# Kernel tuning notes

Measured on AMD Instinct MI355X. Metric: run time of the kernel, lower is better.

The kernel has to match this reference:

```python
import jax, jax.numpy as jnp
import numpy as np
from jax import lax

B, CIN, H, W = 32, 128, 64, 64
COUT, K, NK, HID = 128, 3, 4, 32
TEMP = 34.0
PAD = 1


def setup_inputs() -> dict:
    key = jax.random.key(0)
    k1, k2, k3, k4 = jax.random.split(key, 4)
    x = jax.random.normal(k1, (B, CIN, H, W), dtype=jnp.float32)
    fc1_w = jax.random.normal(k2, (HID, CIN), dtype=jnp.float32) * (2.0 / CIN) ** 0.5
    fc2_w = jax.random.normal(k3, (NK, HID), dtype=jnp.float32) * (2.0 / HID) ** 0.5
    fc2_b = jnp.zeros((NK,), dtype=jnp.float32)
    weight = jax.random.normal(k4, (NK, COUT, CIN, K, K), dtype=jnp.float32) * 0.05
    bias = jnp.zeros((NK, COUT), dtype=jnp.float32)
    return {"x": x, "fc1_w": fc1_w, "fc2_w": fc2_w, "fc2_b": fc2_b,
            "weight": weight, "bias": bias}


def _per_sample_conv(xi, wi):
    # xi: [CIN, H, W], wi: [COUT, CIN, K, K]
    out = lax.conv_general_dilated(
        xi[None], wi,
        window_strides=(1, 1),
        padding=[(PAD, PAD), (PAD, PAD)],
        dimension_numbers=("NCHW", "OIHW", "NCHW"))
    return out[0]  # [COUT, H', W']


def reference(x, fc1_w, fc2_w, fc2_b, weight, bias):
    # attention: global avg pool -> 1x1 conv (matmul) -> relu -> 1x1 conv -> softmax
    context = jnp.mean(x, axis=(2, 3))                      # [B, CIN]
    hid = jax.nn.relu(context @ fc1_w.T)                    # [B, HID]
    logits = hid @ fc2_w.T + fc2_b                          # [B, NK]
    att = jax.nn.softmax(logits / TEMP, axis=1)             # [B, NK]
    # aggregate per-sample kernels and biases
    agg_w = jnp.einsum("bk,koihw->boihw", att, weight)      # [B, COUT, CIN, K, K]
    agg_b = att @ bias                                      # [B, COUT]
    # per-sample convolution (equivalent to the groups=B trick in torch)
    out = jax.vmap(_per_sample_conv)(x, agg_w)              # [B, COUT, H, W]
    return out + agg_b[:, :, None, None]
```

## Files before the change

### kernel.cpp

```cpp
#include <hip/hip_runtime.h>

#define B_    32
#define CIN_  128
#define H_    64
#define W_    64
#define COUT_ 128
#define NK_   4
#define HID_  32
#define TEMP_ 34.0f

typedef short bf16x8 __attribute__((ext_vector_type(8)));
typedef float f32x16 __attribute__((ext_vector_type(16)));

__device__ __forceinline__ short f2bf(float f) {
    union { float f; unsigned u; } c; c.f = f;
    unsigned r = (c.u + 0x7FFFu + ((c.u >> 16) & 1u)) >> 16;
    return (short)r;
}

__global__ __launch_bounds__(64) void k_context(const float* __restrict__ x,
                                                float* __restrict__ ctx) {
    const int bc = blockIdx.x;
    const float* p = x + (size_t)bc * (H_ * W_);
    const int lane = threadIdx.x;
    float s = 0.f;
    for (int i = lane * 4; i < H_ * W_; i += 64 * 4) {
        float4 v = *(const float4*)(p + i);
        s += v.x + v.y + v.z + v.w;
    }
    for (int off = 32; off > 0; off >>= 1) s += __shfl_down(s, off, 64);
    if (lane == 0) ctx[bc] = s * (1.0f / (H_ * W_));
}

__global__ __launch_bounds__(256) void k_aggw(const float* __restrict__ ctx,
        const float* __restrict__ fc1w, const float* __restrict__ fc2w,
        const float* __restrict__ fc2b, const float* __restrict__ bias,
        const float* __restrict__ weight, short* __restrict__ aggwt,
        float* __restrict__ aggb) {
    __shared__ float hidp[8][32];
    __shared__ float shid[32];
    __shared__ float satt[NK_];
    __shared__ float sbuf[2304];
    const int t = threadIdx.x;
    const int blk = blockIdx.x;
    const int b = blk >> 6;
    const int co0 = (blk & 63) * 2;
    {
        const int hh = t & 31, part = t >> 5;
        const float* c  = ctx + b * CIN_ + part * 16;
        const float* f1 = fc1w + hh * CIN_ + part * 16;
        float s = 0.f;
#pragma unroll
        for (int j = 0; j < 16; ++j) s += c[j] * f1[j];
        hidp[part][hh] = s;
    }
    __syncthreads();
    if (t < 32) {
        float s = 0.f;
#pragma unroll
        for (int p = 0; p < 8; ++p) s += hidp[p][t];
        shid[t] = fmaxf(s, 0.f);
    }
    __syncthreads();
    if (t == 0) {
        float lg[NK_]; float mx = -1e30f;
#pragma unroll
        for (int k = 0; k < NK_; ++k) {
            float s = fc2b[k];
            for (int hh = 0; hh < HID_; ++hh) s += shid[hh] * fc2w[k * HID_ + hh];
            lg[k] = s / TEMP_; mx = fmaxf(mx, lg[k]);
        }
        float den = 0.f;
#pragma unroll
        for (int k = 0; k < NK_; ++k) { lg[k] = expf(lg[k] - mx); den += lg[k]; }
        const float rd = 1.0f / den;
#pragma unroll
        for (int k = 0; k < NK_; ++k) satt[k] = lg[k] * rd;
    }
    __syncthreads();
    const float a0 = satt[0], a1 = satt[1], a2 = satt[2], a3 = satt[3];

    if ((t & 127) == 0) {
        const int co = co0 + (t >> 7);
        aggb[b * COUT_ + co] = a0 * bias[co] + a1 * bias[COUT_ + co]
                             + a2 * bias[2 * COUT_ + co] + a3 * bias[3 * COUT_ + co];
    }

    const size_t kstride = (size_t)COUT_ * CIN_ * 9;
    const float* W0 = weight + (size_t)co0 * (CIN_ * 9);
#pragma unroll
    for (int jj = 0; jj < 3; ++jj) {
        const int i4 = jj * 256 + t;
        if (i4 < 576) {
            const float4 w0 = *(const float4*)(W0 + i4 * 4);
            const float4 w1 = *(const float4*)(W0 + kstride + i4 * 4);
            const float4 w2 = *(const float4*)(W0 + 2 * kstride + i4 * 4);
            const float4 w3 = *(const float4*)(W0 + 3 * kstride + i4 * 4);
            float4 r;
            r.x = a0 * w0.x + a1 * w1.x + a2 * w2.x + a3 * w3.x;
            r.y = a0 * w0.y + a1 * w1.y + a2 * w2.y + a3 * w3.y;
            r.z = a0 * w0.z + a1 * w1.z + a2 * w2.z + a3 * w3.z;
            r.w = a0 * w0.w + a1 * w1.w + a2 * w2.w + a3 * w3.w;
            *(float4*)(&sbuf[i4 * 4]) = r;
        }
    }
    __syncthreads();
#pragma unroll
    for (int jj = 0; jj < 2; ++jj) {
        const int g = jj * 256 + t;
        if (g < 288) {
            const int coL = (g >= 144) ? 1 : 0;
            const int gg = g - coL * 144;
            const int r  = gg >> 4;
            const int oc = gg & 15;
            bf16x8 v;
#pragma unroll
            for (int e = 0; e < 8; ++e)
                v[e] = f2bf(sbuf[(coL * 128 + oc * 8 + e) * 9 + r]);
            short* dst = aggwt + ((size_t)(b * COUT_ + co0 + coL) * 9 + r) * CIN_ + oc * 8;
            *(bf16x8*)dst = v;
        }
    }
}

#define RBY2 4352
#define RSH2 2176
__global__ __launch_bounds__(256, 3) void k_conv(const float* __restrict__ x,
        const short* __restrict__ aggwt, const float* __restrict__ aggb,
        float* __restrict__ out) {
    __shared__ short xt[6 * RSH2];
    const int tid = threadIdx.x;
    const int blk = blockIdx.x;
    const int b = blk & 31;
    const int rest = blk >> 5;
    const int h0 = (rest >> 1) * 4;
    const int iw = rest & 1;
    const int lane = tid & 63;
    const int wv = tid >> 6;
    const int l31 = lane & 31;
    const int lane5 = lane >> 5;

    f32x16 acc[4];
#pragma unroll
    for (int t = 0; t < 4; ++t)
#pragma unroll
        for (int k = 0; k < 16; ++k) acc[t][k] = 0.f;

    const short* Ap = aggwt + (size_t)(b * COUT_ + wv * 32 + l31) * 9 * CIN_ + lane5 * 8;

    for (int half = 0; half < 2; ++half) {
        const int cib = half * 64;
#pragma unroll
        for (int k = 0; k < 12; ++k) {
            const int task = k * 4 + wv;
            const int row = task >> 3;
            const int g = task & 7;
            const int in_h = h0 - 1 + row;
            if (lane < 34) {
                const int w = iw * 32 - 1 + lane;
                bf16x8 v = (bf16x8){0, 0, 0, 0, 0, 0, 0, 0};
                if (in_h >= 0 && in_h < H_ && w >= 0 && w < W_) {
                    const float* gp = x + (((size_t)b * CIN_ + cib + g * 8) * H_ + in_h) * W_ + w;
                    float f[8];
#pragma unroll
                    for (int j = 0; j < 8; ++j) f[j] = gp[j * (H_ * W_)];
#pragma unroll
                    for (int j = 0; j < 8; ++j) v[j] = f2bf(f[j]);
                }
                *(bf16x8*)(&xt[row * RSH2 + lane * 64 + ((g + lane - 1) & 7) * 8]) = v;
            }
        }
        __syncthreads();

#pragma unroll
        for (int kcl = 0; kcl < 4; ++kcl) {
            const int kc = half * 4 + kcl;
            bf16x8 av[9];
#pragma unroll
            for (int r = 0; r < 9; ++r)
                av[r] = *(const bf16x8*)(Ap + kc * 16 + r * CIN_);
#pragma unroll
            for (int ir = 0; ir < 6; ++ir) {
                bf16x8 bv[3];
#pragma unroll
                for (int kw = 0; kw < 3; ++kw) {
                    const int s = l31 + kw;
                    const int off = 16 * ((2 * kcl + lane5 + s - 1) & 7);
                    bv[kw] = *(const bf16x8*)((const char*)xt + ir * RBY2 + s * 128 + off);
                }
#pragma unroll
                for (int orr = 0; orr < 4; ++orr) {
                    if (orr <= ir && ir <= orr + 2) {
                        const int kh = ir - orr;
#pragma unroll
                        for (int kw = 0; kw < 3; ++kw)
                            acc[orr] = __builtin_amdgcn_mfma_f32_32x32x16_bf16(
                                av[kh * 3 + kw], bv[kw], acc[orr], 0, 0, 0);
                    }
                }
            }
        }
        if (half == 0) __syncthreads();
    }

    const float* ab = aggb + b * COUT_;
#pragma unroll
    for (int orr = 0; orr < 4; ++orr) {
        const int hh = h0 + orr;
        const int w = iw * 32 + l31;
        float* op = out + ((size_t)b * COUT_ * H_ + hh) * W_ + w;
        const f32x16 a = acc[orr];
#pragma unroll
        for (int reg = 0; reg < 16; ++reg) {
            const int co = wv * 32 + (reg & 3) + 8 * (reg >> 2) + 4 * lane5;
            op[(size_t)co * (H_ * W_)] = a[reg] + ab[co];
        }
    }
}

extern "C" void kernel_launch(void* const* d_in, const int* in_sizes, int n_in,
                              void* d_out, int out_size, void* d_ws, size_t ws_size,
                              hipStream_t stream) {
    const float* x    = (const float*)d_in[0];
    const float* fc1w = (const float*)d_in[1];
    const float* fc2w = (const float*)d_in[2];
    const float* fc2b = (const float*)d_in[3];
    const float* wgt  = (const float*)d_in[4];
    const float* bias = (const float*)d_in[5];
    float* out = (float*)d_out;

    char* ws = (char*)d_ws;
    float* ctx   = (float*)(ws + 0);
    float* aggb  = (float*)(ws + 16384);
    short* aggwt = (short*)(ws + 65536);

    k_context<<<dim3(B_ * CIN_), dim3(64), 0, stream>>>(x, ctx);
    k_aggw<<<dim3(B_ * (COUT_ / 2)), dim3(256), 0, stream>>>(
        ctx, fc1w, fc2w, fc2b, bias, wgt, aggwt, aggb);
    k_conv<<<dim3(B_ * (H_ / 4) * 2), dim3(256), 0, stream>>>(x, aggwt, aggb, out);
}
```

Measured before the change: 191.9 us.

## Widen conv tile to full row width and reorder aggregated weights for coalescing

Each conv block now covers the full 64-wide output rows instead of half, so each A-fragment of aggregated weights feeds twice as many MFMAs and the halo columns are no longer loaded twice. Padding columns are zeroed once up front rather than per staging pass. The aggregated weight buffer is rearranged so each wave's fragment load is contiguous (512-short chunks per tap and channel group). The cost is double the accumulators (8 x f32x16), larger LDS, occupancy lowered to 2 blocks per CU and half as many blocks.

Measured after the change: 169.3 us. -11.8%, faster.

```diff
diff --git a/kernel.cpp b/kernel.cpp
--- a/kernel.cpp
+++ b/kernel.cpp
@@ -113,40 +113,49 @@
             const int gg = g - coL * 144;
             const int r  = gg >> 4;
             const int oc = gg & 15;
+            const int co = co0 + coL;
             bf16x8 v;
 #pragma unroll
             for (int e = 0; e < 8; ++e)
                 v[e] = f2bf(sbuf[(coL * 128 + oc * 8 + e) * 9 + r]);
-            short* dst = aggwt + ((size_t)(b * COUT_ + co0 + coL) * 9 + r) * CIN_ + oc * 8;
+            short* dst = aggwt
+                + ((size_t)(((b * 4 + (co >> 5)) * 9 + r) * 8 + (oc >> 1)) * 512)
+                + ((co & 31) * 2 + (oc & 1)) * 8;
             *(bf16x8*)dst = v;
         }
     }
 }
 
-#define RBY2 4352
-#define RSH2 2176
-__global__ __launch_bounds__(256, 3) void k_conv(const float* __restrict__ x,
+#define RBY 8448
+#define RSH 4224
+__global__ __launch_bounds__(256, 2) void k_conv(const float* __restrict__ x,
         const short* __restrict__ aggwt, const float* __restrict__ aggb,
         float* __restrict__ out) {
-    __shared__ short xt[6 * RSH2];
+    __shared__ short xt[6 * RSH];
     const int tid = threadIdx.x;
     const int blk = blockIdx.x;
     const int b = blk & 31;
-    const int rest = blk >> 5;
-    const int h0 = (rest >> 1) * 4;
-    const int iw = rest & 1;
+    const int h0 = (blk >> 5) * 4;
     const int lane = tid & 63;
     const int wv = tid >> 6;
     const int l31 = lane & 31;
     const int lane5 = lane >> 5;
 
-    f32x16 acc[4];
-#pragma unroll
-    for (int t = 0; t < 4; ++t)
+    if (tid < 96) {
+        const int row = tid >> 4;
+        const int q = tid & 15;
+        const int cl = (q < 8) ? q : (512 + q);
+        *(int4*)(&xt[row * RSH + cl * 8]) = make_int4(0, 0, 0, 0);
+    }
+
+    f32x16 acc[8];
+#pragma unroll
+    for (int t = 0; t < 8; ++t)
 #pragma unroll
         for (int k = 0; k < 16; ++k) acc[t][k] = 0.f;
 
-    const short* Ap = aggwt + (size_t)(b * COUT_ + wv * 32 + l31) * 9 * CIN_ + lane5 * 8;
+    const short* Ap = aggwt + (size_t)(b * 4 + wv) * (9 * 8 * 512)
+                            + (size_t)(l31 * 2 + lane5) * 8;
 
     for (int half = 0; half < 2; ++half) {
         const int cib = half * 64;
@@ -156,19 +165,16 @@
             const int row = task >> 3;
             const int g = task & 7;
             const int in_h = h0 - 1 + row;
-            if (lane < 34) {
-                const int w = iw * 32 - 1 + lane;
-                bf16x8 v = (bf16x8){0, 0, 0, 0, 0, 0, 0, 0};
-                if (in_h >= 0 && in_h < H_ && w >= 0 && w < W_) {
-                    const float* gp = x + (((size_t)b * CIN_ + cib + g * 8) * H_ + in_h) * W_ + w;
-                    float f[8];
-#pragma unroll
-                    for (int j = 0; j < 8; ++j) f[j] = gp[j * (H_ * W_)];
-#pragma unroll
-                    for (int j = 0; j < 8; ++j) v[j] = f2bf(f[j]);
-                }
-                *(bf16x8*)(&xt[row * RSH2 + lane * 64 + ((g + lane - 1) & 7) * 8]) = v;
+            bf16x8 v = (bf16x8){0, 0, 0, 0, 0, 0, 0, 0};
+            if (in_h >= 0 && in_h < H_) {
+                const float* gp = x + (((size_t)b * CIN_ + cib + g * 8) * H_ + in_h) * W_ + lane;
+                float f[8];
+#pragma unroll
+                for (int j = 0; j < 8; ++j) f[j] = gp[j * (H_ * W_)];
+#pragma unroll
+                for (int j = 0; j < 8; ++j) v[j] = f2bf(f[j]);
             }
+            *(bf16x8*)(&xt[row * RSH + ((lane + 1) * 8 + ((g + lane) & 7)) * 8]) = v;
         }
         __syncthreads();
 
@@ -178,24 +184,28 @@
             bf16x8 av[9];
 #pragma unroll
             for (int r = 0; r < 9; ++r)
-                av[r] = *(const bf16x8*)(Ap + kc * 16 + r * CIN_);
+                av[r] = *(const bf16x8*)(Ap + ((size_t)(r * 8 + kc)) * 512);
 #pragma unroll
             for (int ir = 0; ir < 6; ++ir) {
-                bf16x8 bv[3];
-#pragma unroll
-                for (int kw = 0; kw < 3; ++kw) {
-                    const int s = l31 + kw;
-                    const int off = 16 * ((2 * kcl + lane5 + s - 1) & 7);
-                    bv[kw] = *(const bf16x8*)((const char*)xt + ir * RBY2 + s * 128 + off);
-                }
+                bf16x8 bv[2][3];
+#pragma unroll
+                for (int i = 0; i < 2; ++i)
+#pragma unroll
+                    for (int kw = 0; kw < 3; ++kw) {
+                        const int s = i * 32 + l31 + kw;
+                        const int off = 16 * ((2 * kcl + lane5 + s - 1) & 7);
+                        bv[i][kw] = *(const bf16x8*)((const char*)xt + ir * RBY + s * 128 + off);
+                    }
 #pragma unroll
                 for (int orr = 0; orr < 4; ++orr) {
                     if (orr <= ir && ir <= orr + 2) {
                         const int kh = ir - orr;
 #pragma unroll
-                        for (int kw = 0; kw < 3; ++kw)
-                            acc[orr] = __builtin_amdgcn_mfma_f32_32x32x16_bf16(
-                                av[kh * 3 + kw], bv[kw], acc[orr], 0, 0, 0);
+                        for (int i = 0; i < 2; ++i)
+#pragma unroll
+                            for (int kw = 0; kw < 3; ++kw)
+                                acc[orr * 2 + i] = __builtin_amdgcn_mfma_f32_32x32x16_bf16(
+                                    av[kh * 3 + kw], bv[i][kw], acc[orr * 2 + i], 0, 0, 0);
                     }
                 }
             }
@@ -206,14 +216,17 @@
     const float* ab = aggb + b * COUT_;
 #pragma unroll
     for (int orr = 0; orr < 4; ++orr) {
-        const int hh = h0 + orr;
-        const int w = iw * 32 + l31;
-        float* op = out + ((size_t)b * COUT_ * H_ + hh) * W_ + w;
-        const f32x16 a = acc[orr];
-#pragma unroll
-        for (int reg = 0; reg < 16; ++reg) {
-            const int co = wv * 32 + (reg & 3) + 8 * (reg >> 2) + 4 * lane5;
-            op[(size_t)co * (H_ * W_)] = a[reg] + ab[co];
+#pragma unroll
+        for (int i = 0; i < 2; ++i) {
+            const int hh = h0 + orr;
+            const int w = i * 32 + l31;
+            float* op = out + ((size_t)b * COUT_ * H_ + hh) * W_ + w;
+            const f32x16 a = acc[orr * 2 + i];
+#pragma unroll
+            for (int reg = 0; reg < 16; ++reg) {
+                const int co = wv * 32 + (reg & 3) + 8 * (reg >> 2) + 4 * lane5;
+                op[(size_t)co * (H_ * W_)] = a[reg] + ab[co];
+            }
         }
     }
 }
@@ -237,5 +250,5 @@
     k_context<<<dim3(B_ * CIN_), dim3(64), 0, stream>>>(x, ctx);
     k_aggw<<<dim3(B_ * (COUT_ / 2)), dim3(256), 0, stream>>>(
         ctx, fc1w, fc2w, fc2b, bias, wgt, aggwt, aggb);
-    k_conv<<<dim3(B_ * (H_ / 4) * 2), dim3(256), 0, stream>>>(x, aggwt, aggb, out);
-}
+    k_conv<<<dim3(B_ * (H_ / 4)), dim3(256), 0, stream>>>(x, aggwt, aggb, out);
+}
```
